# Optimization experiments

Hardware: AMD Instinct MI355X
Metric: run time of the kernel (lower is better)

The kernel has to match this reference:

```python
import jax, jax.numpy as jnp
import numpy as np

B, L, D = 4, 2048, 512
H, DK = 8, 64          # n_heads, d_k = d_model // n_heads
DF = 2048              # d_ff
W = 9                  # window_size (odd so padding w//2 keeps L windows)


def setup_inputs() -> dict:
    key = jax.random.key(0)
    ks = jax.random.split(key, 12)
    s = 0.02
    p = lambda k, shp: (jax.random.normal(k, shp, jnp.float32) * s)
    return {
        "x": jax.random.normal(ks[0], (B, L, D), jnp.float32),
        "Wq": p(ks[1], (D, D)), "bq": jnp.zeros((D,), jnp.float32),
        "Wk": p(ks[2], (D, D)), "bk": jnp.zeros((D,), jnp.float32),
        "Wv": p(ks[3], (D, D)), "bv": jnp.zeros((D,), jnp.float32),
        "Wo": p(ks[4], (D, D)), "bo": jnp.zeros((D,), jnp.float32),
        "W1": p(ks[5], (D, DF)), "b1": jnp.zeros((DF,), jnp.float32),
        "W2": p(ks[6], (DF, D)), "b2": jnp.zeros((D,), jnp.float32),
        "g1": jnp.ones((D,), jnp.float32), "be1": jnp.zeros((D,), jnp.float32),
        "g2": jnp.ones((D,), jnp.float32), "be2": jnp.zeros((D,), jnp.float32),
    }


def _layer_norm(x, g, b, eps=1e-5):
    m = jnp.mean(x, axis=-1, keepdims=True)
    v = jnp.var(x, axis=-1, keepdims=True)
    return (x - m) * jax.lax.rsqrt(v + eps) * g + b


def reference(x, Wq, bq, Wk, bk, Wv, bv, Wo, bo, W1, b1, W2, b2, g1, be1, g2, be2):
    b, l, d = x.shape
    pad = W // 2
    padded = jnp.pad(x, ((0, 0), (pad, pad), (0, 0)))          # (B, L+W-1, D)
    idx = jnp.arange(l)[:, None] + jnp.arange(W)[None, :]       # (L, W)
    win = padded[:, idx]                                        # (B, L, W, D)

    # per-window full attention (Informer FullAttention, mask_flag=False)
    q = (win @ Wq + bq).reshape(b, l, W, H, DK)
    k = (win @ Wk + bk).reshape(b, l, W, H, DK)
    v = (win @ Wv + bv).reshape(b, l, W, H, DK)
    scale = 1.0 / jnp.sqrt(jnp.float32(DK))
    scores = jnp.einsum('blqhe,blkhe->blhqk', q, k) * scale     # (B, L, H, W, W)
    attn = jax.nn.softmax(scores, axis=-1)
    o = jnp.einsum('blhqk,blkhd->blqhd', attn, v).reshape(b, l, W, d)
    o = o @ Wo + bo                                             # (B, L, W, D)
    new_x = jnp.mean(o, axis=2)                                 # mean-pool over window

    x1 = _layer_norm(x + new_x, g1, be1)

    # pointwise conv FFN (kernel_size=1 Conv1d == Linear), exact GELU
    h = jax.nn.gelu(x1 @ W1 + b1, approximate=False)
    y = h @ W2 + b2
    return _layer_norm(x1 + y, g2, be2)
```

## Files before the change

kernel.cpp:

```cpp
#include <hip/hip_runtime.h>


typedef unsigned short u16;
typedef __attribute__((ext_vector_type(8))) short short8;
typedef __attribute__((ext_vector_type(4))) float floatx4;

#define DEV static __device__ __forceinline__

DEV float b2f(u16 u) {
  union { unsigned int i; float f; } x; x.i = ((unsigned int)u) << 16; return x.f;
}
DEV u16 f2b(float f) {
  union { float f; unsigned int i; } x; x.f = f;
  unsigned int u = x.i + 0x7fffu + ((x.i >> 16) & 1u);
  return (u16)(u >> 16);
}

#define AS1 __attribute__((address_space(1)))
#define AS3 __attribute__((address_space(3)))
DEV void gload_lds16(const void* g, void* l) {
  __builtin_amdgcn_global_load_lds((const AS1 void*)g, (AS3 void*)l, 16, 0, 0);
}

__global__ __launch_bounds__(256) void prep_weights(
    const float* __restrict__ Wq, const float* __restrict__ Wk,
    const float* __restrict__ Wo, const float* __restrict__ W1,
    const float* __restrict__ W2, const float* __restrict__ Wv,
    u16* __restrict__ WqkvT, u16* __restrict__ WoT,
    u16* __restrict__ W1T, u16* __restrict__ W2T, u16* __restrict__ Wvb) {
  const int bid = blockIdx.x;
  if (bid >= 2816) {
    const int i = (bid - 2816) * 256 + threadIdx.x;
    float4 v = ((const float4*)Wv)[i];
    ushort4 o;
    o.x = f2b(v.x); o.y = f2b(v.y); o.z = f2b(v.z); o.w = f2b(v.w);
    ((ushort4*)Wvb)[i] = o;
    return;
  }
  const float* in; u16* out; int R, C, t;
  if (bid < 256)       { in = Wq; out = WqkvT;          R = 512;  C = 512;  t = bid; }
  else if (bid < 512)  { in = Wk; out = WqkvT + 262144; R = 512;  C = 512;  t = bid - 256; }
  else if (bid < 768)  { in = Wo; out = WoT;            R = 512;  C = 512;  t = bid - 512; }
  else if (bid < 1792) { in = W1; out = W1T;            R = 512;  C = 2048; t = bid - 768; }
  else                 { in = W2; out = W2T;            R = 2048; C = 512;  t = bid - 1792; }
  const int tpr = C >> 5;
  const int bc = (t % tpr) * 32, br = (t / tpr) * 32;
  __shared__ float tile[32][33];
  const int tx = threadIdx.x & 31, ty = threadIdx.x >> 5;
  #pragma unroll
  for (int i = 0; i < 32; i += 8)
    tile[ty + i][tx] = in[(size_t)(br + ty + i) * C + bc + tx];
  __syncthreads();
  #pragma unroll
  for (int i = 0; i < 32; i += 8)
    out[(size_t)(bc + ty + i) * R + br + tx] = f2b(tile[tx][ty + i]);
}

__global__ __launch_bounds__(256) void bias_prep(
    const float* __restrict__ bq, const float* __restrict__ bk,
    const float* __restrict__ bv, const float* __restrict__ Wo,
    float* __restrict__ o) {
  const int i = blockIdx.x * 256 + threadIdx.x;
  if (i < 512) o[i] = bq[i];
  else if (i < 1024) o[i] = bk[i - 512];
  else if (i < 1536) {
    const int c = i - 1024;
    float s = 0.f;
    for (int j = 0; j < 512; ++j) s += bv[j] * Wo[(size_t)j * 512 + c];
    o[i] = s;
  } else if (i < 2048) o[i] = 0.f;
}

__global__ __launch_bounds__(256) void f2b_vec(
    const float* __restrict__ in, u16* __restrict__ out, int n4) {
  int i = blockIdx.x * 256 + threadIdx.x;
  if (i < n4) {
    float4 v = ((const float4*)in)[i];
    ushort4 o;
    o.x = f2b(v.x); o.y = f2b(v.y); o.z = f2b(v.z); o.w = f2b(v.w);
    ((ushort4*)out)[i] = o;
  }
}

template<int EPI>
__global__ __launch_bounds__(256, 4) void gemm_bt(
    const u16* __restrict__ A, const u16* __restrict__ BT,
    const float* __restrict__ bias, u16* __restrict__ C, u16* __restrict__ C2,
    int M, int N, int lda, int kb) {
  __shared__ __align__(16) u16 As[3][4096];
  __shared__ __align__(16) u16 Bs[3][2048];
  const int tid = threadIdx.x;
  const int w = tid >> 6, l = tid & 63;
  const int l15 = l & 15, l4 = l >> 4;
  const int wr = w & 1, wc = w >> 1;

  const int gx = (int)gridDim.x, gy = (int)gridDim.y;
  int id = ((int)blockIdx.z * gy + (int)blockIdx.y) * gx + (int)blockIdx.x;
  const int nwg = gx * gy * (int)gridDim.z;
  if ((nwg & 7) == 0) { const int cpx = nwg >> 3; id = (id & 7) * cpx + (id >> 3); }
  const int bx = id % gx; const int r1 = id / gx;
  const int by = r1 % gy; const int bz = r1 / gy;
  const int bm = by * 128, bn = bx * 64;
  const int koff = bz * kb;

  const int row0 = tid >> 2;
  const int kc0 = ((((tid & 3) - ((tid >> 3) & 3)) & 3)) * 8;
  const u16* gA = A  + (size_t)(bm + row0) * lda + koff + kc0;
  const u16* gB = BT + (size_t)(bn + row0) * lda + koff + kc0;
  const size_t a1 = (size_t)64 * lda;
  const int sd = w * 512 + l * 8;

  const int rg8 = ((l4 + ((l15 >> 1) & 3)) & 3) * 8;
  const int aBase = (wr * 64 + l15) * 32 + rg8;
  const int bBase = (wc * 32 + l15) * 32 + rg8;

  floatx4 acc[4][2] = {};
  const int nt = kb >> 5;

  auto stage = [&](int t, int buf) {
    const u16* a = gA + (size_t)t * 32;
    const u16* b = gB + (size_t)t * 32;
    gload_lds16(a,      &As[buf][sd]);
    gload_lds16(a + a1, &As[buf][2048 + sd]);
    gload_lds16(b,      &Bs[buf][sd]);
  };

  stage(0, 0);
  stage(1, 1);
  asm volatile("s_waitcnt vmcnt(3)" ::: "memory");
  __builtin_amdgcn_s_barrier();
  asm volatile("" ::: "memory");

  int cur = 0;
  for (int t = 0; t < nt; ++t) {
    int sb = cur + 2; if (sb >= 3) sb -= 3;
    const bool pf = (t + 2 < nt);
    if (pf) stage(t + 2, sb);

    short8 af[4], bf[2];
    #pragma unroll
    for (int m = 0; m < 4; ++m) af[m] = *(const short8*)(&As[cur][aBase + m * 512]);
    #pragma unroll
    for (int n = 0; n < 2; ++n) bf[n] = *(const short8*)(&Bs[cur][bBase + n * 512]);
    #pragma unroll
    for (int m = 0; m < 4; ++m)
      #pragma unroll
      for (int n = 0; n < 2; ++n)
        acc[m][n] = __builtin_amdgcn_mfma_f32_16x16x32_bf16(af[m], bf[n], acc[m][n], 0, 0, 0);

    if (pf) asm volatile("s_waitcnt vmcnt(3)" ::: "memory");
    else    asm volatile("s_waitcnt vmcnt(0)" ::: "memory");
    __builtin_amdgcn_s_barrier();
    asm volatile("" ::: "memory");

    cur = (cur == 2) ? 0 : cur + 1;
  }

  const int col0 = bn + wc * 32 + l15;
  if (EPI <= 1) {
    float bvv[2];
    #pragma unroll
    for (int n = 0; n < 2; ++n) bvv[n] = bias[col0 + n * 16];
    #pragma unroll
    for (int m = 0; m < 4; ++m) {
      #pragma unroll
      for (int ri = 0; ri < 4; ++ri) {
        const size_t row = (size_t)(bm + wr * 64 + m * 16 + l4 * 4 + ri);
        u16* cp = C + row * N + col0;
        #pragma unroll
        for (int n = 0; n < 2; ++n) {
          float vv = acc[m][n][ri] + bvv[n];
          if (EPI == 1) vv = 0.5f * vv * (1.0f + erff(vv * 0.70710678118654752f));
          cp[n * 16] = f2b(vv);
        }
      }
    }
  } else {
    u16* o = (bz == 0) ? C : C2;
    #pragma unroll
    for (int m = 0; m < 4; ++m) {
      #pragma unroll
      for (int ri = 0; ri < 4; ++ri) {
        const size_t row = (size_t)(bm + wr * 64 + m * 16 + l4 * 4 + ri);
        u16* cp = o + row * N + col0;
        #pragma unroll
        for (int n = 0; n < 2; ++n) cp[n * 16] = f2b(acc[m][n][ri]);
      }
    }
  }
}

#define ATL 32
#define ART (ATL + 8)

__global__ __launch_bounds__(256) void attn_band(
    const u16* __restrict__ QKV, const float* __restrict__ bqkv,
    const float* __restrict__ bo, u16* __restrict__ newx) {
  __shared__ __align__(16) u16 S3[3][ART][72];
  __shared__ float Gb[ART][18];
  __shared__ float Sm[ART][81];
  __shared__ float Wb[ATL][9];

  const int tid = threadIdx.x;
  const int bid = ((int)blockIdx.x & 7) * 256 + ((int)blockIdx.x >> 3);
  const int h = bid & 7;
  const int chunk = (bid >> 3) & 63;
  const int b = bid >> 9;
  const int l0 = chunk * ATL;

  for (int idx = tid; idx < ART * 24; idx += 256) {
    const int ti = idx / 24, c = idx % 24;
    const int slice = c >> 3, d8 = (c & 7) * 8;
    const int col = slice * 512 + h * 64 + d8;
    const int t = l0 - 4 + ti;
    short8 v;
    if ((unsigned)t < 2048u) {
      v = *(const short8*)(QKV + ((size_t)((b << 11) | t)) * 1536 + col);
    } else {
      #pragma unroll
      for (int j = 0; j < 8; ++j) v[j] = (short)f2b(bqkv[col + j]);
    }
    *(short8*)(&S3[slice][ti][d8]) = v;
  }
  __syncthreads();

  for (int task = tid; task < ART * 17; task += 256) {
    const int ti = task / 17, j = task % 17;
    const int ui = ti + j - 8;
    if ((unsigned)ui < (unsigned)ART) {
      float a = 0.f;
      #pragma unroll
      for (int d0 = 0; d0 < 64; d0 += 8) {
        short8 qv = *(const short8*)(&S3[0][ti][d0]);
        short8 kv = *(const short8*)(&S3[1][ui][d0]);
        #pragma unroll
        for (int jj = 0; jj < 8; ++jj) a += b2f((u16)qv[jj]) * b2f((u16)kv[jj]);
      }
      Gb[ti][j] = a * 0.125f;
    }
  }
  __syncthreads();

  for (int task = tid; task < ART * 9; task += 256) {
    const int ti = task / 9, qw = task % 9;
    const int li = ti - qw;
    if ((unsigned)li < (unsigned)ATL) {
      float m = -1e30f;
      #pragma unroll
      for (int kw = 0; kw < 9; ++kw) m = fmaxf(m, Gb[ti][kw - qw + 8]);
      float e[9], s = 0.f;
      #pragma unroll
      for (int kw = 0; kw < 9; ++kw) { e[kw] = expf(Gb[ti][kw - qw + 8] - m); s += e[kw]; }
      const float inv = 1.f / s;
      #pragma unroll
      for (int kw = 0; kw < 9; ++kw) Sm[ti][qw * 9 + kw] = e[kw] * inv;
    }
  }
  __syncthreads();

  for (int task = tid; task < ATL * 9; task += 256) {
    const int li = task / 9, kw = task % 9;
    float s = 0.f;
    #pragma unroll
    for (int qw = 0; qw < 9; ++qw) s += Sm[li + qw][qw * 9 + kw];
    Wb[li][kw] = s * (1.f / 9.f);
  }
  __syncthreads();

  {
    const int li = tid >> 3, d8 = (tid & 7) * 8;
    float w[9];
    #pragma unroll
    for (int kw = 0; kw < 9; ++kw) w[kw] = Wb[li][kw];
    float a[8] = {};
    #pragma unroll
    for (int kw = 0; kw < 9; ++kw) {
      short8 vv = *(const short8*)(&S3[2][li + kw][d8]);
      #pragma unroll
      for (int jj = 0; jj < 8; ++jj) a[jj] += w[kw] * b2f((u16)vv[jj]);
    }
    short8 o;
    #pragma unroll
    for (int jj = 0; jj < 8; ++jj) o[jj] = (short)f2b(a[jj] + bo[h * 64 + d8 + jj]);
    const int l = l0 + li;
    *(short8*)(newx + ((size_t)((b << 11) | l)) * 512 + h * 64 + d8) = o;
  }
}

template<int MODE>
__global__ __launch_bounds__(256) void ln_kernel(
    const u16* __restrict__ a, const u16* __restrict__ bsrc,
    const u16* __restrict__ csrc, const float* __restrict__ bias,
    const float* __restrict__ g, const float* __restrict__ be,
    u16* __restrict__ outb, float* __restrict__ outf) {
  const int wave = threadIdx.x >> 6, lane = threadIdx.x & 63;
  const size_t row = (size_t)blockIdx.x * 4 + wave;
  const size_t base = row * 512 + lane * 8;
  const int gi = lane * 8;
  float v[8];
  short8 a8 = *(const short8*)(a + base);
  short8 b8 = *(const short8*)(bsrc + base);
  #pragma unroll
  for (int j = 0; j < 8; ++j) v[j] = b2f((u16)a8[j]) + b2f((u16)b8[j]);
  if (MODE == 1) {
    short8 c8 = *(const short8*)(csrc + base);
    #pragma unroll
    for (int j = 0; j < 8; ++j) v[j] += b2f((u16)c8[j]) + bias[gi + j];
  }

  float s = 0.f;
  #pragma unroll
  for (int j = 0; j < 8; ++j) s += v[j];
  #pragma unroll
  for (int off = 32; off >= 1; off >>= 1) s += __shfl_xor(s, off, 64);
  const float mean = s * (1.f / 512.f);
  float sq = 0.f;
  #pragma unroll
  for (int j = 0; j < 8; ++j) { float d = v[j] - mean; sq += d * d; }
  #pragma unroll
  for (int off = 32; off >= 1; off >>= 1) sq += __shfl_xor(sq, off, 64);
  const float rs = rsqrtf(sq * (1.f / 512.f) + 1e-5f);

  if (MODE == 0) {
    short8 o;
    #pragma unroll
    for (int j = 0; j < 8; ++j)
      o[j] = (short)f2b((v[j] - mean) * rs * g[gi + j] + be[gi + j]);
    *(short8*)(outb + base) = o;
  } else {
    float4 o0, o1;
    o0.x = (v[0] - mean) * rs * g[gi + 0] + be[gi + 0];
    o0.y = (v[1] - mean) * rs * g[gi + 1] + be[gi + 1];
    o0.z = (v[2] - mean) * rs * g[gi + 2] + be[gi + 2];
    o0.w = (v[3] - mean) * rs * g[gi + 3] + be[gi + 3];
    o1.x = (v[4] - mean) * rs * g[gi + 4] + be[gi + 4];
    o1.y = (v[5] - mean) * rs * g[gi + 5] + be[gi + 5];
    o1.z = (v[6] - mean) * rs * g[gi + 6] + be[gi + 6];
    o1.w = (v[7] - mean) * rs * g[gi + 7] + be[gi + 7];
    *(float4*)(outf + base) = o0;
    *(float4*)(outf + base + 4) = o1;
  }
}

extern "C" void kernel_launch(void* const* d_in, const int* in_sizes, int n_in,
                              void* d_out, int out_size, void* d_ws, size_t ws_size,
                              hipStream_t stream) {
  const float* x   = (const float*)d_in[0];
  const float* Wq  = (const float*)d_in[1];
  const float* bq  = (const float*)d_in[2];
  const float* Wk  = (const float*)d_in[3];
  const float* bk  = (const float*)d_in[4];
  const float* Wv  = (const float*)d_in[5];
  const float* bv  = (const float*)d_in[6];
  const float* Wo  = (const float*)d_in[7];
  const float* bo  = (const float*)d_in[8];
  const float* W1  = (const float*)d_in[9];
  const float* b1  = (const float*)d_in[10];
  const float* W2  = (const float*)d_in[11];
  const float* b2  = (const float*)d_in[12];
  const float* g1  = (const float*)d_in[13];
  const float* be1 = (const float*)d_in[14];
  const float* g2  = (const float*)d_in[15];
  const float* be2 = (const float*)d_in[16];

  char* w = (char*)d_ws;
  u16*   xb    = (u16*)  (w + 0);
  u16*   WqkvT = (u16*)  (w + 8388608);
  u16*   WoT   = (u16*)  (w + 9961472);
  u16*   W1T   = (u16*)  (w + 10485760);
  u16*   W2T   = (u16*)  (w + 12582912);
  float* bqkv  = (float*)(w + 14680064);
  u16*   Wvb   = (u16*)  (w + 14688256);
  u16*   QKV   = (u16*)  (w + 15212544);
  u16*   hbuf  = QKV;
  u16*   newx  = (u16*)  (w + 48766976);
  u16*   x1b   = (u16*)  (w + 57155584);
  u16*   WvoT  = WqkvT + 524288;
  u16*   yp0   = newx;
  u16*   yp1   = xb;

  prep_weights<<<3072, 256, 0, stream>>>(Wq, Wk, Wo, W1, W2, Wv,
                                         WqkvT, WoT, W1T, W2T, Wvb);
  bias_prep<<<8, 256, 0, stream>>>(bq, bk, bv, Wo, bqkv);
  f2b_vec<<<4096, 256, 0, stream>>>(x, xb, 1048576);
  gemm_bt<0><<<dim3(8, 4, 1), 256, 0, stream>>>(WoT, Wvb, bqkv + 1536, WvoT, nullptr,
                                                512, 512, 512, 512);
  gemm_bt<0><<<dim3(24, 64, 1), 256, 0, stream>>>(xb, WqkvT, bqkv, QKV, nullptr,
                                                  8192, 1536, 512, 512);
  attn_band<<<2048, 256, 0, stream>>>(QKV, bqkv, bo, newx);
  ln_kernel<0><<<2048, 256, 0, stream>>>(xb, newx, nullptr, nullptr, g1, be1, x1b, nullptr);
  gemm_bt<1><<<dim3(32, 64, 1), 256, 0, stream>>>(x1b, W1T, b1, hbuf, nullptr,
                                                  8192, 2048, 512, 512);
  gemm_bt<2><<<dim3(8, 64, 2), 256, 0, stream>>>(hbuf, W2T, nullptr, yp0, yp1,
                                                 8192, 512, 2048, 1024);
  ln_kernel<1><<<2048, 256, 0, stream>>>(x1b, yp0, yp1, b2, g2, be2, nullptr, (float*)d_out);
}
```

Baseline: 164.1 us.

## Merge prep kernels, drop split-K for W2 GEMM, use tanh-form GELU

Combines weight transpose, bias preparation and input bf16 conversion into one prep kernel to save launches. Replaces the split-K second FFN GEMM with a single full-K pass that adds b2 in the epilogue, so the final layernorm reads one partial buffer instead of two. Replaces exact erf GELU with a tanh-approximation in sigmoid form using fast exp. This trades parallelism in the W2 GEMM and exactness of GELU for fewer launches and cheaper epilogues.

```diff
diff --git a/kernel.cpp b/kernel.cpp
--- a/kernel.cpp
+++ b/kernel.cpp
@@ -22,13 +22,36 @@
   __builtin_amdgcn_global_load_lds((const AS1 void*)g, (AS3 void*)l, 16, 0, 0);
 }
 
-__global__ __launch_bounds__(256) void prep_weights(
+__global__ __launch_bounds__(256) void prep_all(
     const float* __restrict__ Wq, const float* __restrict__ Wk,
     const float* __restrict__ Wo, const float* __restrict__ W1,
     const float* __restrict__ W2, const float* __restrict__ Wv,
+    const float* __restrict__ bq, const float* __restrict__ bk,
+    const float* __restrict__ bv, const float* __restrict__ x,
     u16* __restrict__ WqkvT, u16* __restrict__ WoT,
-    u16* __restrict__ W1T, u16* __restrict__ W2T, u16* __restrict__ Wvb) {
+    u16* __restrict__ W1T, u16* __restrict__ W2T, u16* __restrict__ Wvb,
+    float* __restrict__ bqkv, u16* __restrict__ xb) {
   const int bid = blockIdx.x;
+  if (bid >= 3080) {
+    const int i = (bid - 3080) * 256 + threadIdx.x;
+    float4 v = ((const float4*)x)[i];
+    ushort4 o;
+    o.x = f2b(v.x); o.y = f2b(v.y); o.z = f2b(v.z); o.w = f2b(v.w);
+    ((ushort4*)xb)[i] = o;
+    return;
+  }
+  if (bid >= 3072) {
+    const int i = (bid - 3072) * 256 + threadIdx.x;
+    if (i < 512) bqkv[i] = bq[i];
+    else if (i < 1024) bqkv[i] = bk[i - 512];
+    else if (i < 1536) {
+      const int c = i - 1024;
+      float s = 0.f;
+      for (int j = 0; j < 512; ++j) s += bv[j] * Wo[(size_t)j * 512 + c];
+      bqkv[i] = s;
+    } else bqkv[i] = 0.f;
+    return;
+  }
   if (bid >= 2816) {
     const int i = (bid - 2816) * 256 + threadIdx.x;
     float4 v = ((const float4*)Wv)[i];
@@ -56,36 +79,10 @@
     out[(size_t)(bc + ty + i) * R + br + tx] = f2b(tile[tx][ty + i]);
 }
 
-__global__ __launch_bounds__(256) void bias_prep(
-    const float* __restrict__ bq, const float* __restrict__ bk,
-    const float* __restrict__ bv, const float* __restrict__ Wo,
-    float* __restrict__ o) {
-  const int i = blockIdx.x * 256 + threadIdx.x;
-  if (i < 512) o[i] = bq[i];
-  else if (i < 1024) o[i] = bk[i - 512];
-  else if (i < 1536) {
-    const int c = i - 1024;
-    float s = 0.f;
-    for (int j = 0; j < 512; ++j) s += bv[j] * Wo[(size_t)j * 512 + c];
-    o[i] = s;
-  } else if (i < 2048) o[i] = 0.f;
-}
-
-__global__ __launch_bounds__(256) void f2b_vec(
-    const float* __restrict__ in, u16* __restrict__ out, int n4) {
-  int i = blockIdx.x * 256 + threadIdx.x;
-  if (i < n4) {
-    float4 v = ((const float4*)in)[i];
-    ushort4 o;
-    o.x = f2b(v.x); o.y = f2b(v.y); o.z = f2b(v.z); o.w = f2b(v.w);
-    ((ushort4*)out)[i] = o;
-  }
-}
-
 template<int EPI>
 __global__ __launch_bounds__(256, 4) void gemm_bt(
     const u16* __restrict__ A, const u16* __restrict__ BT,
-    const float* __restrict__ bias, u16* __restrict__ C, u16* __restrict__ C2,
+    const float* __restrict__ bias, u16* __restrict__ C,
     int M, int N, int lda, int kb) {
   __shared__ __align__(16) u16 As[3][4096];
   __shared__ __align__(16) u16 Bs[3][2048];
@@ -95,18 +92,16 @@
   const int wr = w & 1, wc = w >> 1;
 
   const int gx = (int)gridDim.x, gy = (int)gridDim.y;
-  int id = ((int)blockIdx.z * gy + (int)blockIdx.y) * gx + (int)blockIdx.x;
-  const int nwg = gx * gy * (int)gridDim.z;
+  int id = (int)blockIdx.y * gx + (int)blockIdx.x;
+  const int nwg = gx * gy;
   if ((nwg & 7) == 0) { const int cpx = nwg >> 3; id = (id & 7) * cpx + (id >> 3); }
-  const int bx = id % gx; const int r1 = id / gx;
-  const int by = r1 % gy; const int bz = r1 / gy;
+  const int bx = id % gx; const int by = id / gx;
   const int bm = by * 128, bn = bx * 64;
-  const int koff = bz * kb;
 
   const int row0 = tid >> 2;
   const int kc0 = ((((tid & 3) - ((tid >> 3) & 3)) & 3)) * 8;
-  const u16* gA = A  + (size_t)(bm + row0) * lda + koff + kc0;
-  const u16* gB = BT + (size_t)(bn + row0) * lda + koff + kc0;
+  const u16* gA = A  + (size_t)(bm + row0) * lda + kc0;
+  const u16* gB = BT + (size_t)(bn + row0) * lda + kc0;
   const size_t a1 = (size_t)64 * lda;
   const int sd = w * 512 + l * 8;
 
@@ -157,34 +152,23 @@
   }
 
   const int col0 = bn + wc * 32 + l15;
-  if (EPI <= 1) {
-    float bvv[2];
-    #pragma unroll
-    for (int n = 0; n < 2; ++n) bvv[n] = bias[col0 + n * 16];
-    #pragma unroll
-    for (int m = 0; m < 4; ++m) {
-      #pragma unroll
-      for (int ri = 0; ri < 4; ++ri) {
-        const size_t row = (size_t)(bm + wr * 64 + m * 16 + l4 * 4 + ri);
-        u16* cp = C + row * N + col0;
-        #pragma unroll
-        for (int n = 0; n < 2; ++n) {
-          float vv = acc[m][n][ri] + bvv[n];
-          if (EPI == 1) vv = 0.5f * vv * (1.0f + erff(vv * 0.70710678118654752f));
-          cp[n * 16] = f2b(vv);
+  float bvv[2];
+  #pragma unroll
+  for (int n = 0; n < 2; ++n) bvv[n] = bias[col0 + n * 16];
+  #pragma unroll
+  for (int m = 0; m < 4; ++m) {
+    #pragma unroll
+    for (int ri = 0; ri < 4; ++ri) {
+      const size_t row = (size_t)(bm + wr * 64 + m * 16 + l4 * 4 + ri);
+      u16* cp = C + row * N + col0;
+      #pragma unroll
+      for (int n = 0; n < 2; ++n) {
+        float vv = acc[m][n][ri] + bvv[n];
+        if (EPI == 1) {
+          const float u = vv * (1.0f + 0.044715f * vv * vv);
+          vv = vv / (1.0f + __expf(-1.5957691216057308f * u));
         }
-      }
-    }
-  } else {
-    u16* o = (bz == 0) ? C : C2;
-    #pragma unroll
-    for (int m = 0; m < 4; ++m) {
-      #pragma unroll
-      for (int ri = 0; ri < 4; ++ri) {
-        const size_t row = (size_t)(bm + wr * 64 + m * 16 + l4 * 4 + ri);
-        u16* cp = o + row * N + col0;
-        #pragma unroll
-        for (int n = 0; n < 2; ++n) cp[n * 16] = f2b(acc[m][n][ri]);
+        cp[n * 16] = f2b(vv);
       }
     }
   }
@@ -290,7 +274,6 @@
 template<int MODE>
 __global__ __launch_bounds__(256) void ln_kernel(
     const u16* __restrict__ a, const u16* __restrict__ bsrc,
-    const u16* __restrict__ csrc, const float* __restrict__ bias,
     const float* __restrict__ g, const float* __restrict__ be,
     u16* __restrict__ outb, float* __restrict__ outf) {
   const int wave = threadIdx.x >> 6, lane = threadIdx.x & 63;
@@ -302,11 +285,6 @@
   short8 b8 = *(const short8*)(bsrc + base);
   #pragma unroll
   for (int j = 0; j < 8; ++j) v[j] = b2f((u16)a8[j]) + b2f((u16)b8[j]);
-  if (MODE == 1) {
-    short8 c8 = *(const short8*)(csrc + base);
-    #pragma unroll
-    for (int j = 0; j < 8; ++j) v[j] += b2f((u16)c8[j]) + bias[gi + j];
-  }
 
   float s = 0.f;
   #pragma unroll
@@ -376,22 +354,19 @@
   u16*   newx  = (u16*)  (w + 48766976);
   u16*   x1b   = (u16*)  (w + 57155584);
   u16*   WvoT  = WqkvT + 524288;
-  u16*   yp0   = newx;
-  u16*   yp1   = xb;
-
-  prep_weights<<<3072, 256, 0, stream>>>(Wq, Wk, Wo, W1, W2, Wv,
-                                         WqkvT, WoT, W1T, W2T, Wvb);
-  bias_prep<<<8, 256, 0, stream>>>(bq, bk, bv, Wo, bqkv);
-  f2b_vec<<<4096, 256, 0, stream>>>(x, xb, 1048576);
-  gemm_bt<0><<<dim3(8, 4, 1), 256, 0, stream>>>(WoT, Wvb, bqkv + 1536, WvoT, nullptr,
-                                                512, 512, 512, 512);
-  gemm_bt<0><<<dim3(24, 64, 1), 256, 0, stream>>>(xb, WqkvT, bqkv, QKV, nullptr,
-                                                  8192, 1536, 512, 512);
+  u16*   ybuf  = newx;
+
+  prep_all<<<7176, 256, 0, stream>>>(Wq, Wk, Wo, W1, W2, Wv, bq, bk, bv, x,
+                                     WqkvT, WoT, W1T, W2T, Wvb, bqkv, xb);
+  gemm_bt<0><<<dim3(8, 4), 256, 0, stream>>>(WoT, Wvb, bqkv + 1536, WvoT,
+                                             512, 512, 512, 512);
+  gemm_bt<0><<<dim3(24, 64), 256, 0, stream>>>(xb, WqkvT, bqkv, QKV,
+                                               8192, 1536, 512, 512);
   attn_band<<<2048, 256, 0, stream>>>(QKV, bqkv, bo, newx);
-  ln_kernel<0><<<2048, 256, 0, stream>>>(xb, newx, nullptr, nullptr, g1, be1, x1b, nullptr);
-  gemm_bt<1><<<dim3(32, 64, 1), 256, 0, stream>>>(x1b, W1T, b1, hbuf, nullptr,
-                                                  8192, 2048, 512, 512);
-  gemm_bt<2><<<dim3(8, 64, 2), 256, 0, stream>>>(hbuf, W2T, nullptr, yp0, yp1,
-                                                 8192, 512, 2048, 1024);
-  ln_kernel<1><<<2048, 256, 0, stream>>>(x1b, yp0, yp1, b2, g2, be2, nullptr, (float*)d_out);
-}
+  ln_kernel<0><<<2048, 256, 0, stream>>>(xb, newx, g1, be1, x1b, nullptr);
+  gemm_bt<1><<<dim3(32, 64), 256, 0, stream>>>(x1b, W1T, b1, hbuf,
+                                               8192, 2048, 512, 512);
+  gemm_bt<0><<<dim3(8, 64), 256, 0, stream>>>(hbuf, W2T, b2, ybuf,
+                                              8192, 512, 2048, 2048);
+  ln_kernel<1><<<2048, 256, 0, stream>>>(x1b, ybuf, g2, be2, nullptr, (float*)d_out);
+}
```

After: 165.7 us. No clear change (+1.0%).
